# Performance work log

Hardware: AMD Instinct MI355X
Metric: run time of the kernel (lower is better)

The kernel has to match this reference:

```python
import jax, jax.numpy as jnp
import numpy as np

N_NODES = 100000
N_EDGES = 400000
HIDDEN = 256
N_LAYERS = 4
HEADS = 8
MAX_DEPTH = 20
NUM_GRAPHS = 128
SEQ_LEN = 5
VOCAB = 5002  # vocab_size + 2
NEG_SLOPE = 0.2
BN_EPS = 1e-5


def setup_inputs() -> dict:
    key = jax.random.key(0)
    ks = jax.random.split(key, 16)
    x = jax.random.randint(ks[0], (N_NODES, 2), 0, 98, dtype=jnp.int32)
    node_depth = jax.random.randint(ks[1], (N_NODES, 1), 0, MAX_DEPTH + 1, dtype=jnp.int32)
    edge_index = jax.random.randint(ks[2], (2, N_EDGES), 0, N_NODES, dtype=jnp.int32)
    batch = jnp.sort(jax.random.randint(ks[3], (N_NODES,), 0, NUM_GRAPHS, dtype=jnp.int32))
    s = 1.0 / np.sqrt(HIDDEN)
    return {
        "x": x,
        "node_depth": node_depth,
        "edge_index": edge_index,
        "batch": batch,
        "type_emb": jax.random.normal(ks[4], (98, HIDDEN), jnp.float32) * s,
        "attr_emb": jax.random.normal(ks[5], (10030, HIDDEN), jnp.float32) * s,
        "depth_emb": jax.random.normal(ks[6], (MAX_DEPTH + 1, HIDDEN), jnp.float32) * s,
        "Ws": jax.random.normal(ks[7], (N_LAYERS, HIDDEN, HIDDEN), jnp.float32) * s,
        "att_src": jax.random.normal(ks[8], (N_LAYERS, HIDDEN), jnp.float32) * s,
        "att_dst": jax.random.normal(ks[9], (N_LAYERS, HIDDEN), jnp.float32) * s,
        "gat_bias": jnp.zeros((N_LAYERS, HIDDEN), jnp.float32),
        "bn_gamma": jnp.ones((N_LAYERS, HIDDEN), jnp.float32),
        "bn_beta": jnp.zeros((N_LAYERS, HIDDEN), jnp.float32),
        "tok_W": jax.random.normal(ks[10], (SEQ_LEN, HIDDEN, VOCAB), jnp.float32) * s,
        "tok_b": jnp.zeros((SEQ_LEN, VOCAB), jnp.float32),
    }


def _gat_layer(h, src, dst, W, a_src, a_dst, bias, heads):
    # h: [N, HIDDEN]; PyG GATConv v1 with concat heads, self-loops already in (src, dst)
    N = h.shape[0]
    d = HIDDEN // heads
    hh = (h @ W).reshape(N, heads, d)                       # [N, H, d]
    s_src = jnp.einsum("nhd,hd->nh", hh, a_src.reshape(heads, d))
    s_dst = jnp.einsum("nhd,hd->nh", hh, a_dst.reshape(heads, d))
    e = jax.nn.leaky_relu(s_src[src] + s_dst[dst], NEG_SLOPE)  # [E, H]
    m = jax.ops.segment_max(e, dst, num_segments=N)           # [N, H]
    ex = jnp.exp(e - m[dst])
    denom = jax.ops.segment_sum(ex, dst, num_segments=N)      # [N, H]
    alpha = ex / denom[dst]                                    # [E, H]
    msg = hh[src] * alpha[:, :, None]                          # [E, H, d]
    out = jax.ops.segment_sum(msg, dst, num_segments=N)       # [N, H, d]
    return out.reshape(N, HIDDEN) + bias


def _batchnorm(h, gamma, beta):
    mu = jnp.mean(h, axis=0)
    var = jnp.var(h, axis=0)
    return (h - mu) * jax.lax.rsqrt(var + BN_EPS) * gamma + beta


def reference(x, node_depth, edge_index, batch, type_emb, attr_emb, depth_emb,
              Ws, att_src, att_dst, gat_bias, bn_gamma, bn_beta, tok_W, tok_b):
    N = x.shape[0]
    depth = jnp.minimum(node_depth.reshape(-1), MAX_DEPTH)
    h = type_emb[x[:, 0]] + attr_emb[x[:, 1]] + depth_emb[depth]  # [N, HIDDEN]

    # add self loops (PyG GATConv default)
    loop = jnp.arange(N, dtype=edge_index.dtype)
    src = jnp.concatenate([edge_index[0], loop])
    dst = jnp.concatenate([edge_index[1], loop])

    heads_per_layer = [HEADS] * (N_LAYERS - 1) + [1]
    for l in range(N_LAYERS):
        identity = h
        h = _gat_layer(h, src, dst, Ws[l], att_src[l], att_dst[l], gat_bias[l], heads_per_layer[l])
        h = _batchnorm(h, bn_gamma[l], bn_beta[l])
        h = jax.nn.relu(h)
        h = h + identity  # residual

    # mean pool per graph
    counts = jax.ops.segment_sum(jnp.ones((N,), h.dtype), batch, num_segments=NUM_GRAPHS)
    g = jax.ops.segment_sum(h, batch, num_segments=NUM_GRAPHS) / jnp.maximum(counts, 1.0)[:, None]

    # seq_len token predictors -> [SEQ_LEN, G, VOCAB]
    preds = jnp.einsum("gh,shv->sgv", g, tok_W) + tok_b[:, None, :]
    return preds
```

## Files before the change

### kernel.cpp

```cpp
#include <hip/hip_runtime.h>
#include <stdint.h>

typedef uint16_t u16;
typedef uint32_t u32;

#define N_NODESC 100000
#define N_EDGESC 400000
#define E_TOT    500000
#define HID      256
#define NLAYERS  4
#define NGRAPHS  128
#define SEQLEN   5
#define VOCABC   5002
#define MAXDEPTH 20
#define NEG_SLOPE 0.2f
#define BN_EPSC  1e-5f
#define NCHUNK   ((N_NODESC + 255)/256)
#define NCH64    ((N_NODESC + 63)/64)
#define NROWT    (N_NODESC/16)
#define NPART    64
#define NVQ      ((VOCABC + 63)/64)
#define ATTNB    2048
#define LDSROW   264

typedef __attribute__((ext_vector_type(8))) short short8;
typedef __attribute__((ext_vector_type(4))) float f32x4;
typedef __attribute__((ext_vector_type(4))) unsigned short u16x4;

__device__ __forceinline__ float b2f(u16 u){
  union { u32 i; float f; } v; v.i = ((u32)u) << 16; return v.f;
}
__device__ __forceinline__ u16 f2b(float f){
  union { float f; u32 i; } v; v.f = f;
  u32 u = v.i;
  u += 0x7FFFu + ((u >> 16) & 1u);
  return (u16)(u >> 16);
}
__device__ __forceinline__ float ldp(const void* p, size_t i, int f){
  return f ? ((const float*)p)[i] : b2f(((const u16*)p)[i]);
}
__device__ __forceinline__ f32x4 ld4(const void* p, size_t i, int f){
  f32x4 r;
  if (f){
    r = *(const f32x4*)((const float*)p + i);
  } else {
    const u16x4 u = *(const u16x4*)((const u16*)p + i);
    r[0] = b2f(u[0]); r[1] = b2f(u[1]); r[2] = b2f(u[2]); r[3] = b2f(u[3]);
  }
  return r;
}

__global__ __launch_bounds__(64) void k_detect(const void* temb, int* flag){
  int lane = threadIdx.x;
  const u32* w32 = (const u32*)temb;
  int sf = 0, sb = 0;
  for (int i = lane; i < 256; i += 64){
    u32 w = w32[i];
    union { u32 u; float f; } cf; cf.u = w;
    float af = fabsf(cf.f);
    if (cf.f == 0.0f || (af >= 1e-12f && af <= 4096.f)) sf++;
    float b0 = b2f((u16)(w & 0xFFFFu));
    float b1 = b2f((u16)(w >> 16));
    float a0 = fabsf(b0), a1 = fabsf(b1);
    if (b0 == 0.f || (a0 >= 1e-12f && a0 <= 4096.f)) sb++;
    if (b1 == 0.f || (a1 >= 1e-12f && a1 <= 4096.f)) sb++;
  }
  #pragma unroll
  for (int o = 1; o < 64; o <<= 1){ sf += __shfl_xor(sf, o); sb += __shfl_xor(sb, o); }
  if (lane == 0) *flag = (2*sf > sb) ? 1 : 0;
}

__global__ __launch_bounds__(256) void k_zero(int* __restrict__ p, int n){
  int i = blockIdx.x*256 + threadIdx.x;
  if (i < n) p[i] = 0;
}

__global__ __launch_bounds__(256) void k_embed(const int* __restrict__ x, const int* __restrict__ nd,
    const void* __restrict__ temb, const void* __restrict__ aemb, const void* __restrict__ demb,
    u16* __restrict__ h, const int* __restrict__ flagp, int* __restrict__ cursor){
  int f = *flagp;
  int tid = threadIdx.x;
  int r0 = blockIdx.x*64;
  if (tid < 64 && r0 + tid < N_NODESC) cursor[r0 + tid] = 0;
  int wid = tid >> 6, lane = tid & 63;
  int c4 = lane*4;
  #pragma unroll 4
  for (int k = 0; k < 16; ++k){
    int n = r0 + wid*16 + k;
    if (n >= N_NODESC) break;
    int t = x[n*2+0], a = x[n*2+1];
    if (t < 0) t = 0; if (t > 97) t = 97;
    if (a < 0) a = 0; if (a > 10029) a = 10029;
    int d = nd[n]; if (d > MAXDEPTH) d = MAXDEPTH; if (d < 0) d = 0;
    const f32x4 vt = ld4(temb, (size_t)t*HID + c4, f);
    const f32x4 va = ld4(aemb, (size_t)a*HID + c4, f);
    const f32x4 vd = ld4(demb, (size_t)d*HID + c4, f);
    u16x4 o;
    #pragma unroll
    for (int j = 0; j < 4; ++j) o[j] = f2b(vt[j] + va[j] + vd[j]);
    *(u16x4*)(h + (size_t)n*HID + c4) = o;
  }
}

__global__ __launch_bounds__(256) void k_hist(const int* __restrict__ ei, int* __restrict__ cnt){
  int e = blockIdx.x*256 + threadIdx.x;
  if (e >= E_TOT) return;
  int dst = (e < N_EDGESC) ? ei[N_EDGESC + e] : (e - N_EDGESC);
  if ((unsigned)dst >= N_NODESC) return;
  atomicAdd(&cnt[dst], 1);
}

__global__ __launch_bounds__(256) void k_scan_part(const int* __restrict__ cnt,
    int* __restrict__ off, int* __restrict__ btot){
  __shared__ int lds[256];
  int b = blockIdx.x, tid = threadIdx.x;
  int i = b*256 + tid;
  int v = (i < N_NODESC) ? cnt[i] : 0;
  lds[tid] = v;
  __syncthreads();
  #pragma unroll
  for (int s = 1; s < 256; s <<= 1){
    int t = (tid >= s) ? lds[tid - s] : 0;
    __syncthreads();
    lds[tid] += t;
    __syncthreads();
  }
  if (i < N_NODESC) off[i] = lds[tid] - v;
  if (tid == 255) btot[b] = lds[255];
}

__global__ __launch_bounds__(256) void k_scan_tot(const int* __restrict__ btot,
    int* __restrict__ boff, int* __restrict__ offN){
  __shared__ int lds[256];
  __shared__ int s_carry;
  int tid = threadIdx.x;
  if (tid == 0) s_carry = 0;
  __syncthreads();
  for (int base = 0; base < NCHUNK; base += 256){
    int i = base + tid;
    int v = (i < NCHUNK) ? btot[i] : 0;
    lds[tid] = v;
    __syncthreads();
    #pragma unroll
    for (int s = 1; s < 256; s <<= 1){
      int t = (tid >= s) ? lds[tid - s] : 0;
      __syncthreads();
      lds[tid] += t;
      __syncthreads();
    }
    if (i < NCHUNK) boff[i] = s_carry + lds[tid] - v;
    __syncthreads();
    if (tid == 255) s_carry += lds[255];
    __syncthreads();
  }
  if (tid == 0) *offN = s_carry;
}

__global__ __launch_bounds__(256) void k_scan_add(int* __restrict__ off,
    const int* __restrict__ boff, int* __restrict__ cursor){
  int b = blockIdx.x;
  int i = b*256 + threadIdx.x;
  if (i < N_NODESC){ off[i] += boff[b]; cursor[i] = 0; }
}

__global__ __launch_bounds__(256) void k_scatter(const int* __restrict__ ei,
    const int* __restrict__ soff, int* __restrict__ cursor, int* __restrict__ ssorted){
  int e = blockIdx.x*256 + threadIdx.x;
  if (e >= E_TOT) return;
  int src = (e < N_EDGESC) ? ei[e]            : (e - N_EDGESC);
  int dst = (e < N_EDGESC) ? ei[N_EDGESC + e] : (e - N_EDGESC);
  if ((unsigned)dst >= N_NODESC || (unsigned)src >= N_NODESC) return;
  int pos = soff[dst] + atomicAdd(&cursor[dst], 1);
  if ((unsigned)pos < E_TOT) ssorted[pos] = src;
}

__global__ __launch_bounds__(256) void k_transW(const void* __restrict__ W, u16* __restrict__ WT,
    const int* __restrict__ flagp){
  int f = *flagp;
  int l = blockIdx.y, n2 = blockIdx.x, k = threadIdx.x;
  WT[(l*HID + n2)*HID + k] = f2b(ldp(W, (size_t)(l*HID + k)*HID + n2, f));
}

__global__ __launch_bounds__(256) void k_prepVA(const void* __restrict__ Ws,
    const void* __restrict__ asrc, const void* __restrict__ adst,
    u16* __restrict__ VAT, const int* __restrict__ flagp){
  int f = *flagp;
  int l = blockIdx.x;
  int i = threadIdx.x;
  int H = (l == NLAYERS-1) ? 1 : 8;
  float col[16];
  #pragma unroll
  for (int c = 0; c < 16; ++c) col[c] = 0.f;
  if (H == 8){
    for (int h = 0; h < 8; ++h){
      float vs = 0.f, vd = 0.f;
      for (int o = h*32; o < h*32+32; ++o){
        float w = ldp(Ws, ((size_t)l*HID + i)*HID + o, f);
        vs += w * ldp(asrc, (size_t)l*HID + o, f);
        vd += w * ldp(adst, (size_t)l*HID + o, f);
      }
      col[h*2] = vs; col[h*2+1] = vd;
    }
  } else {
    float vs = 0.f, vd = 0.f;
    for (int o = 0; o < HID; ++o){
      float w = ldp(Ws, ((size_t)l*HID + i)*HID + o, f);
      vs += w * ldp(asrc, (size_t)l*HID + o, f);
      vd += w * ldp(adst, (size_t)l*HID + o, f);
    }
    col[0] = vs; col[1] = vd;
  }
  #pragma unroll
  for (int c = 0; c < 16; ++c)
    VAT[((size_t)l*16 + c)*HID + i] = f2b(col[c]);
}

__global__ __launch_bounds__(256) void k_gemm(u16* __restrict__ h,
    const u16* __restrict__ gout, const float* __restrict__ scale,
    const float* __restrict__ shift, int doApply,
    const u16* __restrict__ WT, const u16* __restrict__ VAT,
    u16* __restrict__ hh, float* __restrict__ ssrc, float* __restrict__ sdst,
    int H, float* __restrict__ bnpart){
  __shared__ u16 hA[16*LDSROW];
  int tid = threadIdx.x;
  if (blockIdx.x < NPART*2) bnpart[blockIdx.x*256 + tid] = 0.f;
  int wave = tid >> 6, lane = tid & 63;
  int m = lane & 15, quad = lane >> 4;
  int prow = tid >> 4, pch = (tid & 15)*16;

  short8 B[4][8];
  #pragma unroll
  for (int j = 0; j < 4; ++j){
    const u16* wp = WT + (size_t)((wave*4 + j)*16 + m)*HID + quad*8;
    #pragma unroll
    for (int ks = 0; ks < 8; ++ks)
      B[j][ks] = *(const short8*)(wp + ks*32);
  }
  short8 B5[8];
  if (wave == 0){
    const u16* vp = VAT + (size_t)m*HID + quad*8;
    #pragma unroll
    for (int ks = 0; ks < 8; ++ks)
      B5[ks] = *(const short8*)(vp + ks*32);
  }

  for (int t = blockIdx.x; t < NROWT; t += gridDim.x){
    int r0 = t*16;
    {
      size_t base = (size_t)(r0 + prow)*HID + pch;
      short8 h0 = *(const short8*)(h + base);
      short8 h1 = *(const short8*)(h + base + 8);
      if (doApply){
        const short8 g0 = *(const short8*)(gout + base);
        const short8 g1 = *(const short8*)(gout + base + 8);
        #pragma unroll
        for (int v = 0; v < 2; ++v){
          const f32x4 sc = *(const f32x4*)(scale + pch + v*4);
          const f32x4 sh = *(const f32x4*)(shift + pch + v*4);
          #pragma unroll
          for (int j = 0; j < 4; ++j){
            float tv = b2f((u16)g0[v*4+j])*sc[j] + sh[j];
            tv = (tv > 0.f) ? tv : 0.f;
            h0[v*4+j] = (short)f2b(b2f((u16)h0[v*4+j]) + tv);
          }
        }
        #pragma unroll
        for (int v = 0; v < 2; ++v){
          const f32x4 sc = *(const f32x4*)(scale + pch + 8 + v*4);
          const f32x4 sh = *(const f32x4*)(shift + pch + 8 + v*4);
          #pragma unroll
          for (int j = 0; j < 4; ++j){
            float tv = b2f((u16)g1[v*4+j])*sc[j] + sh[j];
            tv = (tv > 0.f) ? tv : 0.f;
            h1[v*4+j] = (short)f2b(b2f((u16)h1[v*4+j]) + tv);
          }
        }
        *(short8*)(h + base)     = h0;
        *(short8*)(h + base + 8) = h1;
      }
      *(short8*)(&hA[prow*LDSROW + pch])     = h0;
      *(short8*)(&hA[prow*LDSROW + pch + 8]) = h1;
    }
    __syncthreads();

    short8 A[8];
    #pragma unroll
    for (int ks = 0; ks < 8; ++ks)
      A[ks] = *(const short8*)(&hA[m*LDSROW + ks*32 + quad*8]);

    f32x4 acc[4];
    #pragma unroll
    for (int j = 0; j < 4; ++j) acc[j] = (f32x4){0.f,0.f,0.f,0.f};
    #pragma unroll
    for (int ks = 0; ks < 8; ++ks){
      #pragma unroll
      for (int j = 0; j < 4; ++j)
        acc[j] = __builtin_amdgcn_mfma_f32_16x16x32_bf16(A[ks], B[j][ks], acc[j], 0, 0, 0);
    }

    if (wave == 0){
      f32x4 acc5 = (f32x4){0.f,0.f,0.f,0.f};
      #pragma unroll
      for (int ks = 0; ks < 8; ++ks)
        acc5 = __builtin_amdgcn_mfma_f32_16x16x32_bf16(A[ks], B5[ks], acc5, 0, 0, 0);
      int hidx = m >> 1, sd = m & 1;
      #pragma unroll
      for (int r = 0; r < 4; ++r){
        int row = r0 + quad*4 + r;
        float val = acc5[r];
        if (H == 8){
          if (sd == 0) ssrc[row*8 + hidx] = val;
          else         sdst[row*8 + hidx] = val;
        } else {
          if (m == 0)      ssrc[row] = val;
          else if (m == 1) sdst[row] = val;
        }
      }
    }

    #pragma unroll
    for (int j = 0; j < 4; ++j){
      int col = (wave*4 + j)*16 + m;
      #pragma unroll
      for (int r = 0; r < 4; ++r){
        int orow = r0 + quad*4 + r;
        hh[(size_t)orow*HID + col] = f2b(acc[j][r]);
      }
    }
    __syncthreads();
  }
}

__device__ __forceinline__ void attn_node(int n, int lane, const u16* __restrict__ hh,
    const float* __restrict__ ssrc, const float* __restrict__ sdst,
    const int* __restrict__ soff, const int* __restrict__ ssorted, int H, float r[4]){
  int f0 = lane*4;
  int hl = (H == 8) ? (lane >> 3) : 0;
  float sd = sdst[n*H + hl];
  int beg = soff[n], end = soff[n+1];
  if (beg < 0) beg = 0;
  if (end > E_TOT) end = E_TOT;
  r[0] = r[1] = r[2] = r[3] = 0.f;
  if (beg >= end) return;
  int src = ssorted[beg];
  if ((unsigned)src >= N_NODESC) src = n;
  u16x4 hvv = *(const u16x4*)(hh + (size_t)src*HID + f0);
  float es = ssrc[src*H + hl];
  float lval = 0.f;
  float o0 = 0.f, o1 = 0.f, o2 = 0.f, o3 = 0.f;
  for (int i = beg; i < end; ++i){
    int nsrc = src;
    if (i + 1 < end){
      nsrc = ssorted[i+1];
      if ((unsigned)nsrc >= N_NODESC) nsrc = src;
    }
    const u16x4 nh = *(const u16x4*)(hh + (size_t)nsrc*HID + f0);
    const float nes = ssrc[nsrc*H + hl];
    float ev = es + sd;
    ev = (ev > 0.f) ? ev : NEG_SLOPE*ev;
    ev = fminf(fmaxf(ev, -60.f), 60.f);
    float wv = __expf(ev);
    lval += wv;
    o0 += wv*b2f(hvv[0]);
    o1 += wv*b2f(hvv[1]);
    o2 += wv*b2f(hvv[2]);
    o3 += wv*b2f(hvv[3]);
    hvv = nh; es = nes;
  }
  float inv = (lval > 0.f) ? 1.f/lval : 0.f;
  r[0] = o0*inv; r[1] = o1*inv; r[2] = o2*inv; r[3] = o3*inv;
}

__global__ __launch_bounds__(256) void k_attn_gout(const u16* __restrict__ hh,
    const float* __restrict__ ssrc, const float* __restrict__ sdst,
    const int* __restrict__ soff, const int* __restrict__ ssorted,
    u16* __restrict__ gout, int H, float* __restrict__ bnpart){
  __shared__ float lsum[4*HID];
  __shared__ float lsq[4*HID];
  int wid = threadIdx.x >> 6, lane = threadIdx.x & 63;
  int f0 = lane*4;
  float s[4] = {0.f,0.f,0.f,0.f}, q[4] = {0.f,0.f,0.f,0.f};
  int gw = blockIdx.x*4 + wid;
  int nw = gridDim.x*4;
  for (int n = gw; n < N_NODESC; n += nw){
    float r[4];
    attn_node(n, lane, hh, ssrc, sdst, soff, ssorted, H, r);
    u16x4 o;
    #pragma unroll
    for (int j = 0; j < 4; ++j){
      o[j] = f2b(r[j]);
      s[j] += r[j];
      q[j] += r[j]*r[j];
    }
    *(u16x4*)(gout + (size_t)n*HID + f0) = o;
  }
  #pragma unroll
  for (int j = 0; j < 4; ++j){
    lsum[wid*HID + f0 + j] = s[j];
    lsq [wid*HID + f0 + j] = q[j];
  }
  __syncthreads();
  int c = threadIdx.x;
  float ts = lsum[c] + lsum[HID+c] + lsum[2*HID+c] + lsum[3*HID+c];
  float tq = lsq[c]  + lsq[HID+c]  + lsq[2*HID+c]  + lsq[3*HID+c];
  float* prow = bnpart + (size_t)(blockIdx.x & (NPART-1))*512;
  atomicAdd(&prow[c], ts);
  atomicAdd(&prow[HID + c], tq);
}

__global__ __launch_bounds__(256) void k_attn_stats(const u16* __restrict__ hh,
    const float* __restrict__ ssrc, const float* __restrict__ sdst,
    const int* __restrict__ soff, const int* __restrict__ ssorted,
    float* __restrict__ bnpart, int H){
  __shared__ float lsum[4*HID];
  __shared__ float lsq[4*HID];
  int wid = threadIdx.x >> 6, lane = threadIdx.x & 63;
  int gw = blockIdx.x*4 + wid;
  int nw = gridDim.x*4;
  float s[4] = {0.f,0.f,0.f,0.f}, q[4] = {0.f,0.f,0.f,0.f};
  for (int n = gw; n < N_NODESC; n += nw){
    float r[4];
    attn_node(n, lane, hh, ssrc, sdst, soff, ssorted, H, r);
    #pragma unroll
    for (int j = 0; j < 4; ++j){ s[j] += r[j]; q[j] += r[j]*r[j]; }
  }
  int f0 = lane*4;
  #pragma unroll
  for (int j = 0; j < 4; ++j){ lsum[wid*HID + f0 + j] = s[j]; lsq[wid*HID + f0 + j] = q[j]; }
  __syncthreads();
  int c = threadIdx.x;
  float ts = lsum[c] + lsum[HID+c] + lsum[2*HID+c] + lsum[3*HID+c];
  float tq = lsq[c]  + lsq[HID+c]  + lsq[2*HID+c]  + lsq[3*HID+c];
  float* prow = bnpart + (size_t)(blockIdx.x & (NPART-1))*512;
  atomicAdd(&prow[c], ts);
  atomicAdd(&prow[HID + c], tq);
}

__global__ __launch_bounds__(256) void k_attn_apply(const u16* __restrict__ hh,
    const float* __restrict__ ssrc, const float* __restrict__ sdst,
    const int* __restrict__ soff, const int* __restrict__ ssorted,
    const float* __restrict__ scale, const float* __restrict__ shift,
    u16* __restrict__ h, int H){
  int wid = threadIdx.x >> 6, lane = threadIdx.x & 63;
  int n = blockIdx.x*4 + wid;
  if (n >= N_NODESC) return;
  float r[4];
  attn_node(n, lane, hh, ssrc, sdst, soff, ssorted, H, r);
  int f0 = lane*4;
  const f32x4 sc = *(const f32x4*)(scale + f0);
  const f32x4 sh = *(const f32x4*)(shift + f0);
  u16x4 hv = *(u16x4*)(h + (size_t)n*HID + f0);
  u16x4 o;
  #pragma unroll
  for (int j = 0; j < 4; ++j){
    float t = r[j]*sc[j] + sh[j];
    t = (t > 0.f) ? t : 0.f;
    o[j] = f2b(b2f(hv[j]) + t);
  }
  *(u16x4*)(h + (size_t)n*HID + f0) = o;
}

__global__ __launch_bounds__(256) void k_bn_final(const float* __restrict__ bnpart,
    const void* __restrict__ gamma, const void* __restrict__ beta,
    float* __restrict__ scale, float* __restrict__ shift,
    const int* __restrict__ flagp, int loff){
  int f = *flagp;
  int c = threadIdx.x;
  float s = 0.f, q = 0.f;
  #pragma unroll 4
  for (int p = 0; p < NPART; ++p){
    s += bnpart[(size_t)p*512 + c];
    q += bnpart[(size_t)p*512 + HID + c];
  }
  float mu  = s * (1.f/N_NODESC);
  float var = q * (1.f/N_NODESC) - mu*mu;
  if (!(var >= 0.f)) var = 0.f;
  float sc = ldp(gamma, (size_t)loff + c, f) * rsqrtf(var + BN_EPSC);
  scale[c] = sc;
  shift[c] = ldp(beta, (size_t)loff + c, f) - mu*sc;
}

__global__ __launch_bounds__(256) void k_pool(const u16* __restrict__ h,
    const int* __restrict__ batch, float* __restrict__ gsum, int* __restrict__ gcnt){
  int c = threadIdx.x;
  int r0 = blockIdx.x * 256;
  int r1 = min(r0 + 256, N_NODESC);
  if (r0 >= N_NODESC) return;
  int cur = batch[r0];
  float acc = 0.f;
  int nacc = 0;
  for (int r = r0; r < r1; ++r){
    int b = batch[r];
    if ((unsigned)b >= NGRAPHS) continue;
    if (b != cur){
      if ((unsigned)cur < NGRAPHS){
        atomicAdd(&gsum[cur*HID + c], acc);
        if (c == 0) atomicAdd(&gcnt[cur], nacc);
      }
      acc = 0.f; nacc = 0; cur = b;
    }
    acc += b2f(h[(size_t)r*HID + c]);
    nacc++;
  }
  if ((unsigned)cur < NGRAPHS){
    atomicAdd(&gsum[cur*HID + c], acc);
    if (c == 0) atomicAdd(&gcnt[cur], nacc);
  }
}

__global__ __launch_bounds__(256) void k_pool_fused(const u16* __restrict__ h,
    const u16* __restrict__ gout, const float* __restrict__ scale, const float* __restrict__ shift,
    const int* __restrict__ batch, float* __restrict__ gsum, int* __restrict__ gcnt){
  __shared__ int lb[64];
  int tid = threadIdx.x;
  int r0 = blockIdx.x*64;
  if (tid < 64){
    int rr = r0 + tid;
    lb[tid] = (rr < N_NODESC) ? batch[rr] : -1;
  }
  __syncthreads();
  int wid = tid >> 6, lane = tid & 63;
  int c4 = lane*4;
  const f32x4 sc = *(const f32x4*)(scale + c4);
  const f32x4 sh = *(const f32x4*)(shift + c4);
  int rbase = r0 + wid*16;
  f32x4 acc = (f32x4){0.f,0.f,0.f,0.f};
  int nacc = 0, cur = -1;
  #pragma unroll 4
  for (int k = 0; k < 16; ++k){
    int r = rbase + k;
    if (r >= N_NODESC) break;
    int b = lb[wid*16 + k];
    if ((unsigned)b >= NGRAPHS) continue;
    if (b != cur){
      if ((unsigned)cur < NGRAPHS){
        atomicAdd(&gsum[cur*HID + c4+0], acc[0]);
        atomicAdd(&gsum[cur*HID + c4+1], acc[1]);
        atomicAdd(&gsum[cur*HID + c4+2], acc[2]);
        atomicAdd(&gsum[cur*HID + c4+3], acc[3]);
        if (lane == 0) atomicAdd(&gcnt[cur], nacc);
      }
      acc = (f32x4){0.f,0.f,0.f,0.f}; nacc = 0; cur = b;
    }
    const u16x4 hv = *(const u16x4*)(h    + (size_t)r*HID + c4);
    const u16x4 gv = *(const u16x4*)(gout + (size_t)r*HID + c4);
    #pragma unroll
    for (int j = 0; j < 4; ++j){
      float t = b2f(gv[j])*sc[j] + sh[j];
      t = (t > 0.f) ? t : 0.f;
      acc[j] += b2f(hv[j]) + t;
    }
    nacc++;
  }
  if ((unsigned)cur < NGRAPHS){
    atomicAdd(&gsum[cur*HID + c4+0], acc[0]);
    atomicAdd(&gsum[cur*HID + c4+1], acc[1]);
    atomicAdd(&gsum[cur*HID + c4+2], acc[2]);
    atomicAdd(&gsum[cur*HID + c4+3], acc[3]);
    if (lane == 0) atomicAdd(&gcnt[cur], nacc);
  }
}

__global__ __launch_bounds__(256) void k_gprep(const float* __restrict__ gsum,
    const int* __restrict__ gcnt, u16* __restrict__ gbf){
  int g = blockIdx.x, c = threadIdx.x;
  int cc = gcnt[g]; if (cc < 1) cc = 1;
  gbf[g*HID + c] = f2b(gsum[(size_t)g*HID + c] * (1.f/(float)cc));
}

__global__ __launch_bounds__(256) void k_pred(const u16* __restrict__ gbf,
    const void* __restrict__ tokW, const void* __restrict__ tokb, void* __restrict__ out,
    const int* __restrict__ flagp){
  int f = *flagp;
  int wave = threadIdx.x >> 6, lane = threadIdx.x & 63;
  int m = lane & 15, quad = lane >> 4;
  int s = blockIdx.y;
  int v = blockIdx.x*64 + wave*16 + m;
  bool vok = (v < VOCABC);

  f32x4 acc[8];
  #pragma unroll
  for (int t = 0; t < 8; ++t) acc[t] = (f32x4){0.f,0.f,0.f,0.f};

  const size_t wrow = (size_t)s*HID*VOCABC + v;
  #pragma unroll
  for (int ks = 0; ks < 8; ++ks){
    int kb = ks*32 + quad*8;
    short8 b;
    #pragma unroll
    for (int j = 0; j < 8; ++j)
      b[j] = vok ? (short)f2b(ldp(tokW, wrow + (size_t)(kb + j)*VOCABC, f)) : (short)0;
    #pragma unroll
    for (int t = 0; t < 8; ++t){
      const short8 a = *(const short8*)(gbf + (size_t)(t*16 + m)*HID + kb);
      acc[t] = __builtin_amdgcn_mfma_f32_16x16x32_bf16(a, b, acc[t], 0, 0, 0);
    }
  }

  float bb = vok ? ldp(tokb, (size_t)s*VOCABC + v, f) : 0.f;
  if (!vok) return;
  #pragma unroll
  for (int t = 0; t < 8; ++t){
    #pragma unroll
    for (int r = 0; r < 4; ++r){
      int grow = t*16 + quad*4 + r;
      float val = acc[t][r] + bb;
      size_t oi = ((size_t)(s*NGRAPHS + grow)*VOCABC) + v;
      if (f) ((float*)out)[oi] = val;
      else   ((u16*)out)[oi]   = f2b(val);
    }
  }
}

extern "C" void kernel_launch(void* const* d_in, const int* in_sizes, int n_in,
                              void* d_out, int out_size, void* d_ws, size_t ws_size,
                              hipStream_t stream) {
  const int* x          = (const int*)d_in[0];
  const int* node_depth = (const int*)d_in[1];
  const int* edge_index = (const int*)d_in[2];
  const int* batch      = (const int*)d_in[3];
  const void* type_emb  = d_in[4];
  const void* attr_emb  = d_in[5];
  const void* depth_emb = d_in[6];
  const void* Ws        = d_in[7];
  const void* att_src   = d_in[8];
  const void* att_dst   = d_in[9];
  const void* bn_gamma  = d_in[11];
  const void* bn_beta   = d_in[12];
  const void* tok_W     = d_in[13];
  const void* tok_b     = d_in[14];

  char* base = (char*)d_ws;
  size_t off = 0;
  auto carve = [&](size_t bytes) -> void* {
    void* p = base + off;
    off += (bytes + 255) & ~(size_t)255;
    return p;
  };
  u16*   h     = (u16*)carve((size_t)N_NODESC*HID*2);
  u16*   hh    = (u16*)carve((size_t)N_NODESC*HID*2);
  float* ssrc  = (float*)carve((size_t)N_NODESC*8*4);
  float* sdst  = (float*)carve((size_t)N_NODESC*8*4);
  int*   soff  = (int*)carve((size_t)(N_NODESC+1)*4);
  int*   cursor= (int*)carve((size_t)N_NODESC*4);
  int*   ssorted=(int*)carve((size_t)E_TOT*4);
  int*   btot  = (int*)carve((size_t)NCHUNK*4);
  int*   boff  = (int*)carve((size_t)NCHUNK*4);
  u16*   WT    = (u16*)carve((size_t)NLAYERS*HID*HID*2);
  u16*   VAT   = (u16*)carve((size_t)NLAYERS*16*HID*2);
  float* bnpart= (float*)carve((size_t)NPART*512*4);
  float* bnscale=(float*)carve(HID*4);
  float* bnshift=(float*)carve(HID*4);
  float* gsum  = (float*)carve((size_t)NGRAPHS*HID*4);
  int*   gcnt  = (int*)carve((size_t)NGRAPHS*4);
  u16*   gbf   = (u16*)carve((size_t)NGRAPHS*HID*2);
  int*   dflag = (int*)carve(256);
  size_t common = off;
  u16*   gout  = (u16*)carve((size_t)N_NODESC*HID*2);
  const bool useGout = (off <= ws_size);
  if (common > ws_size) return;

  const int EB  = (E_TOT + 255)/256;
  const int NB4 = (N_NODESC + 3)/4;

  k_detect<<<1, 64, 0, stream>>>(type_emb, dflag);

  k_embed<<<NCH64, 256, 0, stream>>>(x, node_depth, type_emb, attr_emb, depth_emb, h, dflag, cursor);
  k_transW<<<dim3(256, NLAYERS), 256, 0, stream>>>(Ws, WT, dflag);
  k_prepVA<<<NLAYERS, 256, 0, stream>>>(Ws, att_src, att_dst, VAT, dflag);
  k_hist<<<EB, 256, 0, stream>>>(edge_index, cursor);
  k_scan_part<<<NCHUNK, 256, 0, stream>>>(cursor, soff, btot);
  k_scan_tot<<<1, 256, 0, stream>>>(btot, boff, soff + N_NODESC);
  k_scan_add<<<NCHUNK, 256, 0, stream>>>(soff, boff, cursor);
  k_scatter<<<EB, 256, 0, stream>>>(edge_index, soff, cursor, ssorted);

  for (int l = 0; l < NLAYERS; ++l){
    int H = (l == NLAYERS-1) ? 1 : 8;
    int doApply = (useGout && l > 0) ? 1 : 0;
    k_gemm<<<1024, 256, 0, stream>>>(h, gout, bnscale, bnshift, doApply,
                                     WT + (size_t)l*HID*HID, VAT + (size_t)l*16*HID,
                                     hh, ssrc, sdst, H, bnpart);
    if (useGout){
      k_attn_gout<<<ATTNB, 256, 0, stream>>>(hh, ssrc, sdst, soff, ssorted, gout, H, bnpart);
      k_bn_final<<<1, 256, 0, stream>>>(bnpart, bn_gamma, bn_beta, bnscale, bnshift, dflag, l*HID);
    } else {
      k_attn_stats<<<2048, 256, 0, stream>>>(hh, ssrc, sdst, soff, ssorted, bnpart, H);
      k_bn_final<<<1, 256, 0, stream>>>(bnpart, bn_gamma, bn_beta, bnscale, bnshift, dflag, l*HID);
      k_attn_apply<<<NB4, 256, 0, stream>>>(hh, ssrc, sdst, soff, ssorted, bnscale, bnshift, h, H);
    }
  }

  k_zero<<<(NGRAPHS*HID + NGRAPHS + 255)/256, 256, 0, stream>>>((int*)gsum, NGRAPHS*HID + NGRAPHS);
  if (useGout)
    k_pool_fused<<<NCH64, 256, 0, stream>>>(h, gout, bnscale, bnshift, batch, gsum, gcnt);
  else
    k_pool<<<NCHUNK, 256, 0, stream>>>(h, batch, gsum, gcnt);
  k_gprep<<<NGRAPHS, 256, 0, stream>>>(gsum, gcnt, gbf);

  k_pred<<<dim3(NVQ, SEQLEN), 256, 0, stream>>>(gbf, tok_W, tok_b, d_out, dflag);
}
```

Baseline: 834.0 us.

## Double-buffer GEMM row tiles and prefetch next tile's inputs in registers

The per-layer GEMM kernel now uses two LDS buffers for the 16-row A tile and issues global loads for the next tile's h/gout rows before the MFMA work on the current tile. This removes the trailing __syncthreads and lets global latency overlap with compute. BN scale/shift vectors are also hoisted out of the loop into registers. The cost is higher register pressure and extra LDS, plus a raw s_barrier with manual lgkmcnt wait instead of __syncthreads.

```diff
diff --git a/kernel.cpp b/kernel.cpp
--- a/kernel.cpp
+++ b/kernel.cpp
@@ -221,7 +221,7 @@
     const u16* __restrict__ WT, const u16* __restrict__ VAT,
     u16* __restrict__ hh, float* __restrict__ ssrc, float* __restrict__ sdst,
     int H, float* __restrict__ bnpart){
-  __shared__ u16 hA[16*LDSROW];
+  __shared__ u16 hA[2][16*LDSROW];
   int tid = threadIdx.x;
   if (blockIdx.x < NPART*2) bnpart[blockIdx.x*256 + tid] = 0.f;
   int wave = tid >> 6, lane = tid & 63;
@@ -244,49 +244,85 @@
       B5[ks] = *(const short8*)(vp + ks*32);
   }
 
-  for (int t = blockIdx.x; t < NROWT; t += gridDim.x){
-    int r0 = t*16;
+  f32x4 sc0 = {}, sc1 = {}, sc2 = {}, sc3 = {};
+  f32x4 sh0 = {}, sh1 = {}, sh2 = {}, sh3 = {};
+  if (doApply){
+    sc0 = *(const f32x4*)(scale + pch);      sh0 = *(const f32x4*)(shift + pch);
+    sc1 = *(const f32x4*)(scale + pch + 4);  sh1 = *(const f32x4*)(shift + pch + 4);
+    sc2 = *(const f32x4*)(scale + pch + 8);  sh2 = *(const f32x4*)(shift + pch + 8);
+    sc3 = *(const f32x4*)(scale + pch + 12); sh3 = *(const f32x4*)(shift + pch + 12);
+  }
+
+  int t = blockIdx.x;
+  if (t >= NROWT) return;
+
+  short8 h0, h1, g0 = {}, g1 = {};
+  {
+    size_t base = (size_t)(t*16 + prow)*HID + pch;
+    h0 = *(const short8*)(h + base);
+    h1 = *(const short8*)(h + base + 8);
+    if (doApply){
+      g0 = *(const short8*)(gout + base);
+      g1 = *(const short8*)(gout + base + 8);
+    }
+  }
+
+  int p = 0;
+  for (;;){
     {
-      size_t base = (size_t)(r0 + prow)*HID + pch;
-      short8 h0 = *(const short8*)(h + base);
-      short8 h1 = *(const short8*)(h + base + 8);
+      size_t base = (size_t)(t*16 + prow)*HID + pch;
       if (doApply){
-        const short8 g0 = *(const short8*)(gout + base);
-        const short8 g1 = *(const short8*)(gout + base + 8);
         #pragma unroll
-        for (int v = 0; v < 2; ++v){
-          const f32x4 sc = *(const f32x4*)(scale + pch + v*4);
-          const f32x4 sh = *(const f32x4*)(shift + pch + v*4);
-          #pragma unroll
-          for (int j = 0; j < 4; ++j){
-            float tv = b2f((u16)g0[v*4+j])*sc[j] + sh[j];
-            tv = (tv > 0.f) ? tv : 0.f;
-            h0[v*4+j] = (short)f2b(b2f((u16)h0[v*4+j]) + tv);
-          }
+        for (int j = 0; j < 4; ++j){
+          float tv = b2f((u16)g0[j])*sc0[j] + sh0[j];
+          tv = (tv > 0.f) ? tv : 0.f;
+          h0[j] = (short)f2b(b2f((u16)h0[j]) + tv);
         }
         #pragma unroll
-        for (int v = 0; v < 2; ++v){
-          const f32x4 sc = *(const f32x4*)(scale + pch + 8 + v*4);
-          const f32x4 sh = *(const f32x4*)(shift + pch + 8 + v*4);
-          #pragma unroll
-          for (int j = 0; j < 4; ++j){
-            float tv = b2f((u16)g1[v*4+j])*sc[j] + sh[j];
-            tv = (tv > 0.f) ? tv : 0.f;
-            h1[v*4+j] = (short)f2b(b2f((u16)h1[v*4+j]) + tv);
-          }
+        for (int j = 0; j < 4; ++j){
+          float tv = b2f((u16)g0[4+j])*sc1[j] + sh1[j];
+          tv = (tv > 0.f) ? tv : 0.f;
+          h0[4+j] = (short)f2b(b2f((u16)h0[4+j]) + tv);
+        }
+        #pragma unroll
+        for (int j = 0; j < 4; ++j){
+          float tv = b2f((u16)g1[j])*sc2[j] + sh2[j];
+          tv = (tv > 0.f) ? tv : 0.f;
+          h1[j] = (short)f2b(b2f((u16)h1[j]) + tv);
+        }
+        #pragma unroll
+        for (int j = 0; j < 4; ++j){
+          float tv = b2f((u16)g1[4+j])*sc3[j] + sh3[j];
+          tv = (tv > 0.f) ? tv : 0.f;
+          h1[4+j] = (short)f2b(b2f((u16)h1[4+j]) + tv);
         }
         *(short8*)(h + base)     = h0;
         *(short8*)(h + base + 8) = h1;
       }
-      *(short8*)(&hA[prow*LDSROW + pch])     = h0;
-      *(short8*)(&hA[prow*LDSROW + pch + 8]) = h1;
-    }
-    __syncthreads();
+      *(short8*)(&hA[p][prow*LDSROW + pch])     = h0;
+      *(short8*)(&hA[p][prow*LDSROW + pch + 8]) = h1;
+    }
+
+    int tn = t + gridDim.x;
+    bool hn = (tn < NROWT);
+    short8 nh0 = h0, nh1 = h1, ng0 = g0, ng1 = g1;
+    if (hn){
+      size_t nbase = (size_t)(tn*16 + prow)*HID + pch;
+      nh0 = *(const short8*)(h + nbase);
+      nh1 = *(const short8*)(h + nbase + 8);
+      if (doApply){
+        ng0 = *(const short8*)(gout + nbase);
+        ng1 = *(const short8*)(gout + nbase + 8);
+      }
+    }
+
+    asm volatile("s_waitcnt lgkmcnt(0)" ::: "memory");
+    __builtin_amdgcn_s_barrier();
 
     short8 A[8];
     #pragma unroll
     for (int ks = 0; ks < 8; ++ks)
-      A[ks] = *(const short8*)(&hA[m*LDSROW + ks*32 + quad*8]);
+      A[ks] = *(const short8*)(&hA[p][m*LDSROW + ks*32 + quad*8]);
 
     f32x4 acc[4];
     #pragma unroll
@@ -298,6 +334,7 @@
         acc[j] = __builtin_amdgcn_mfma_f32_16x16x32_bf16(A[ks], B[j][ks], acc[j], 0, 0, 0);
     }
 
+    int r0 = t*16;
     if (wave == 0){
       f32x4 acc5 = (f32x4){0.f,0.f,0.f,0.f};
       #pragma unroll
@@ -327,7 +364,10 @@
         hh[(size_t)orow*HID + col] = f2b(acc[j][r]);
       }
     }
-    __syncthreads();
+
+    if (!hn) break;
+    t = tn; p ^= 1;
+    h0 = nh0; h1 = nh1; g0 = ng0; g1 = ng1;
   }
 }
 
```

Result: faster. 798.1 us (-4.3%).
